# Performance work log

Measured on AMD Instinct MI355X. Metric: run time of the kernel, lower is better.

## Reference

```python
import jax, jax.numpy as jnp
import numpy as np

B, S, IN, OUT = 16, 512, 1024, 4096
QMAX = 127.0

def setup_inputs() -> dict:
    key = jax.random.key(0)
    k1, k2, k3, k4 = jax.random.split(key, 4)
    x = jax.random.normal(k1, (B, S, IN), dtype=jnp.float32)
    # int8 weights stored as int32 spec but clamped to int8 range, cast to int8
    weight_int8 = jax.random.randint(k2, (OUT, IN), -128, 128, dtype=jnp.int32).astype(jnp.int8)
    weight_scale = jax.random.uniform(k3, (OUT,), dtype=jnp.float32, minval=1e-4, maxval=0.02)
    bias = jax.random.normal(k4, (OUT,), dtype=jnp.float32)
    return {"x": x, "weight_int8": weight_int8, "weight_scale": weight_scale, "bias": bias}

def reference(x, weight_int8, weight_scale, bias):
    # dynamic per-token abs-max quantization
    abs_max = jnp.max(jnp.abs(x), axis=-1, keepdims=True)          # [B,S,1]
    input_scale = abs_max / QMAX
    input_scale = jnp.where(input_scale == 0, 1.0, input_scale)
    x_int8 = jnp.clip(jnp.round(x / input_scale), -128.0, 127.0)   # float-emulated int8
    # int8 matmul emulated in float (as in the original F.linear on .float())
    out_i32 = jnp.einsum('bsi,oi->bso', x_int8, weight_int8.astype(jnp.float32))
    out = out_i32 * weight_scale * input_scale                     # dequantize
    out = out + bias
    return out
```

## Files before the change

kernel.cpp:

```cpp
#include <hip/hip_runtime.h>


#define M_TOT 8192
#define N_TOT 4096
#define K_TOT 1024
#define QMAXF 127.0f

#define BM 256
#define BN 256
#define BK 128
#define NKT (K_TOT / BK)

typedef int i32x4 __attribute__((ext_vector_type(4)));

__global__ __launch_bounds__(256) void prep(const float* __restrict__ x,
                                            const int* __restrict__ w32,
                                            signed char* __restrict__ xq,
                                            signed char* __restrict__ w8,
                                            float* __restrict__ iscale) {
  const int b = blockIdx.x;
  const int t = threadIdx.x;

  if (b < M_TOT) {
    const float4 v = reinterpret_cast<const float4*>(x)[(size_t)b * 256 + t];
    float m = fmaxf(fmaxf(fabsf(v.x), fabsf(v.y)), fmaxf(fabsf(v.z), fabsf(v.w)));
#pragma unroll
    for (int off = 32; off >= 1; off >>= 1) m = fmaxf(m, __shfl_xor(m, off, 64));

    __shared__ float wmax[4];
    const int lane = t & 63, wid = t >> 6;
    if (lane == 0) wmax[wid] = m;
    __syncthreads();
    const float amax = fmaxf(fmaxf(wmax[0], wmax[1]), fmaxf(wmax[2], wmax[3]));

    float scale = amax / QMAXF;
    if (scale == 0.0f) scale = 1.0f;

    int qi;
    signed char* qb = reinterpret_cast<signed char*>(&qi);
    qb[0] = (signed char)(int)fminf(fmaxf(rintf(v.x / scale), -128.0f), 127.0f);
    qb[1] = (signed char)(int)fminf(fmaxf(rintf(v.y / scale), -128.0f), 127.0f);
    qb[2] = (signed char)(int)fminf(fmaxf(rintf(v.z / scale), -128.0f), 127.0f);
    qb[3] = (signed char)(int)fminf(fmaxf(rintf(v.w / scale), -128.0f), 127.0f);
    reinterpret_cast<int*>(xq)[(size_t)b * 256 + t] = qi;

    if (t == 0) iscale[b] = scale;
  } else {
    const int i = (b - M_TOT) * 256 + t;
    const int4 v = reinterpret_cast<const int4*>(w32)[i];
    const int packed = (v.x & 0xFF) | ((v.y & 0xFF) << 8) |
                       ((v.z & 0xFF) << 16) | (v.w << 24);
    reinterpret_cast<int*>(w8)[i] = packed;
  }
}

__device__ __forceinline__ void gload_lds16(const void* g, void* l) {
  __builtin_amdgcn_global_load_lds(
      (const __attribute__((address_space(1))) unsigned int*)g,
      (__attribute__((address_space(3))) unsigned int*)l, 16, 0, 0);
}

__global__ __launch_bounds__(512, 2) void int8_gemm(const signed char* __restrict__ xq,
                                                    const signed char* __restrict__ w,
                                                    const float* __restrict__ iscale,
                                                    const float* __restrict__ wscale,
                                                    const float* __restrict__ bias,
                                                    float* __restrict__ out) {
  __shared__ __attribute__((aligned(16))) signed char As[2][BM][BK];
  __shared__ __attribute__((aligned(16))) signed char Bs[2][BN][BK];

  const int t = threadIdx.x;
  const int lane = t & 63;
  const int wid = t >> 6;
  const int wm = wid >> 2;
  const int wn = wid & 3;

  const int bid = blockIdx.x;
  const int swz = (bid & 7) * 64 + (bid >> 3);
  const int m0 = (swz >> 4) * BM;
  const int n0 = (swz & 15) * BN;

  const int srow = t >> 3;
  const int scol_swz = ((t & 7) * 16) ^ ((srow & 7) << 4);

  auto stage = [&](int buf, int kt) {
    const int k0 = kt * BK;
#pragma unroll
    for (int c = 0; c < 4; ++c) {
      gload_lds16(xq + (size_t)(m0 + c * 64 + srow) * K_TOT + k0 + scol_swz,
                  &As[buf][c * 64][0] + t * 16);
      gload_lds16(w + (size_t)(n0 + c * 64 + srow) * K_TOT + k0 + scol_swz,
                  &Bs[buf][c * 64][0] + t * 16);
    }
  };

  i32x4 acc[8][4] = {};

  stage(0, 0);
  __syncthreads();

  for (int kt = 0; kt < NKT; ++kt) {
    const int cur = kt & 1;
    if (kt + 1 < NKT) stage(cur ^ 1, kt + 1);

#pragma unroll
    for (int ks = 0; ks < 2; ++ks) {
      const int kofs = ks * 64 + ((lane >> 4) * 16);
      i32x4 a[8], b[4];
#pragma unroll
      for (int f = 0; f < 8; ++f) {
        const int r = wm * 128 + f * 16 + (lane & 15);
        a[f] = *reinterpret_cast<const i32x4*>(&As[cur][r][kofs ^ ((r & 7) << 4)]);
      }
#pragma unroll
      for (int g = 0; g < 4; ++g) {
        const int r = wn * 64 + g * 16 + (lane & 15);
        b[g] = *reinterpret_cast<const i32x4*>(&Bs[cur][r][kofs ^ ((r & 7) << 4)]);
      }
#pragma unroll
      for (int f = 0; f < 8; ++f)
#pragma unroll
        for (int g = 0; g < 4; ++g)
          acc[f][g] = __builtin_amdgcn_mfma_i32_16x16x64_i8(a[f], b[g], acc[f][g], 0, 0, 0);
    }
    __syncthreads();
  }

  const int col = lane & 15;
  const int rq = lane >> 4;
  float wsc[4], bv[4];
#pragma unroll
  for (int g = 0; g < 4; ++g) {
    const int gn = n0 + wn * 64 + g * 16 + col;
    wsc[g] = wscale[gn];
    bv[g] = bias[gn];
  }
#pragma unroll
  for (int f = 0; f < 8; ++f) {
    const int gmb = m0 + wm * 128 + f * 16 + rq * 4;
#pragma unroll
    for (int i = 0; i < 4; ++i) {
      const int gm = gmb + i;
      const float isc = iscale[gm];
      float* rowp = out + (size_t)gm * N_TOT + n0 + wn * 64 + col;
#pragma unroll
      for (int g = 0; g < 4; ++g)
        rowp[g * 16] = (float)acc[f][g][i] * wsc[g] * isc + bv[g];
    }
  }
}

extern "C" void kernel_launch(void* const* d_in, const int* in_sizes, int n_in,
                              void* d_out, int out_size, void* d_ws, size_t ws_size,
                              hipStream_t stream) {
  const float* x = (const float*)d_in[0];
  const int* w32 = (const int*)d_in[1];
  const float* wscale = (const float*)d_in[2];
  const float* bias = (const float*)d_in[3];
  float* out = (float*)d_out;

  signed char* xq = (signed char*)d_ws;
  float* iscale = (float*)((char*)d_ws + (size_t)M_TOT * K_TOT);
  signed char* w8 = (signed char*)((char*)d_ws + (size_t)M_TOT * K_TOT + M_TOT * 4);

  const int pack_blocks = (N_TOT * K_TOT / 4) / 256;
  prep<<<M_TOT + pack_blocks, 256, 0, stream>>>(x, w32, xq, w8, iscale);
  int8_gemm<<<dim3((M_TOT / BM) * (N_TOT / BN)), 512, 0, stream>>>(xq, w8, iscale, wscale, bias, out);
}
```

Measured before the change: 63.93 us.

## Drop LDS staging; load MFMA operands directly from global into registers

Replaces the LDS double-buffered 256x256 tile GEMM with a register-only scheme. Each wave loads its A/B fragments straight from global memory into registers, double-buffered across k-steps, with s_setprio around the MFMA bursts. Block tile becomes 128x256 with 4 waves, and the grid mapping is remapped per XCD. Output stores become nontemporal. This removes LDS traffic and barriers, but every wave loses operand sharing through LDS and relies on L1/L2 for reuse, which raises global load traffic.

```diff
diff --git a/kernel.cpp b/kernel.cpp
--- a/kernel.cpp
+++ b/kernel.cpp
@@ -5,11 +5,6 @@
 #define N_TOT 4096
 #define K_TOT 1024
 #define QMAXF 127.0f
-
-#define BM 256
-#define BN 256
-#define BK 128
-#define NKT (K_TOT / BK)
 
 typedef int i32x4 __attribute__((ext_vector_type(4)));
 
@@ -54,76 +49,54 @@
   }
 }
 
-__device__ __forceinline__ void gload_lds16(const void* g, void* l) {
-  __builtin_amdgcn_global_load_lds(
-      (const __attribute__((address_space(1))) unsigned int*)g,
-      (__attribute__((address_space(3))) unsigned int*)l, 16, 0, 0);
-}
+#define LOADK(A_, B_, kt)                                                      \
+  _Pragma("unroll") for (int f = 0; f < 8; ++f)                                \
+      A_[f] = *reinterpret_cast<const i32x4*>(Abase + f * 16 * K_TOT + (kt) * 64); \
+  _Pragma("unroll") for (int g = 0; g < 4; ++g)                                \
+      B_[g] = *reinterpret_cast<const i32x4*>(Bbase + g * 16 * K_TOT + (kt) * 64);
 
-__global__ __launch_bounds__(512, 2) void int8_gemm(const signed char* __restrict__ xq,
+#define MFMAS(A_, B_)                                                          \
+  __builtin_amdgcn_s_setprio(1);                                               \
+  _Pragma("unroll") for (int f = 0; f < 8; ++f)                                \
+  _Pragma("unroll") for (int g = 0; g < 4; ++g)                                \
+      acc[f][g] = __builtin_amdgcn_mfma_i32_16x16x64_i8(A_[f], B_[g],          \
+                                                        acc[f][g], 0, 0, 0);   \
+  __builtin_amdgcn_s_setprio(0);
+
+__global__ __launch_bounds__(256, 2) void int8_gemm(const signed char* __restrict__ xq,
                                                     const signed char* __restrict__ w,
                                                     const float* __restrict__ iscale,
                                                     const float* __restrict__ wscale,
                                                     const float* __restrict__ bias,
                                                     float* __restrict__ out) {
-  __shared__ __attribute__((aligned(16))) signed char As[2][BM][BK];
-  __shared__ __attribute__((aligned(16))) signed char Bs[2][BN][BK];
-
   const int t = threadIdx.x;
   const int lane = t & 63;
   const int wid = t >> 6;
-  const int wm = wid >> 2;
-  const int wn = wid & 3;
 
   const int bid = blockIdx.x;
-  const int swz = (bid & 7) * 64 + (bid >> 3);
-  const int m0 = (swz >> 4) * BM;
-  const int n0 = (swz & 15) * BN;
+  const int xcd = bid & 7, li = bid >> 3;
+  const int mt = (xcd >> 1) * 16 + (li >> 3);
+  const int nt = (xcd & 1) * 8 + (li & 7);
+  const int m0 = mt * 128;
+  const int n0 = nt * 256 + wid * 64;
 
-  const int srow = t >> 3;
-  const int scol_swz = ((t & 7) * 16) ^ ((srow & 7) << 4);
-
-  auto stage = [&](int buf, int kt) {
-    const int k0 = kt * BK;
-#pragma unroll
-    for (int c = 0; c < 4; ++c) {
-      gload_lds16(xq + (size_t)(m0 + c * 64 + srow) * K_TOT + k0 + scol_swz,
-                  &As[buf][c * 64][0] + t * 16);
-      gload_lds16(w + (size_t)(n0 + c * 64 + srow) * K_TOT + k0 + scol_swz,
-                  &Bs[buf][c * 64][0] + t * 16);
-    }
-  };
+  const int lr = lane & 15;
+  const int kq = (lane >> 4) * 16;
+  const signed char* Abase = xq + (size_t)(m0 + lr) * K_TOT + kq;
+  const signed char* Bbase = w + (size_t)(n0 + lr) * K_TOT + kq;
 
   i32x4 acc[8][4] = {};
+  i32x4 a0[8], b0[4], a1[8], b1[4];
 
-  stage(0, 0);
-  __syncthreads();
-
-  for (int kt = 0; kt < NKT; ++kt) {
-    const int cur = kt & 1;
-    if (kt + 1 < NKT) stage(cur ^ 1, kt + 1);
+  LOADK(a0, b0, 0)
+  LOADK(a1, b1, 1)
 
 #pragma unroll
-    for (int ks = 0; ks < 2; ++ks) {
-      const int kofs = ks * 64 + ((lane >> 4) * 16);
-      i32x4 a[8], b[4];
-#pragma unroll
-      for (int f = 0; f < 8; ++f) {
-        const int r = wm * 128 + f * 16 + (lane & 15);
-        a[f] = *reinterpret_cast<const i32x4*>(&As[cur][r][kofs ^ ((r & 7) << 4)]);
-      }
-#pragma unroll
-      for (int g = 0; g < 4; ++g) {
-        const int r = wn * 64 + g * 16 + (lane & 15);
-        b[g] = *reinterpret_cast<const i32x4*>(&Bs[cur][r][kofs ^ ((r & 7) << 4)]);
-      }
-#pragma unroll
-      for (int f = 0; f < 8; ++f)
-#pragma unroll
-        for (int g = 0; g < 4; ++g)
-          acc[f][g] = __builtin_amdgcn_mfma_i32_16x16x64_i8(a[f], b[g], acc[f][g], 0, 0, 0);
-    }
-    __syncthreads();
+  for (int kt = 0; kt < K_TOT / 64; kt += 2) {
+    MFMAS(a0, b0)
+    if (kt + 2 < K_TOT / 64) LOADK(a0, b0, kt + 2)
+    MFMAS(a1, b1)
+    if (kt + 3 < K_TOT / 64) LOADK(a1, b1, kt + 3)
   }
 
   const int col = lane & 15;
@@ -131,21 +104,22 @@
   float wsc[4], bv[4];
 #pragma unroll
   for (int g = 0; g < 4; ++g) {
-    const int gn = n0 + wn * 64 + g * 16 + col;
+    const int gn = n0 + g * 16 + col;
     wsc[g] = wscale[gn];
     bv[g] = bias[gn];
   }
 #pragma unroll
   for (int f = 0; f < 8; ++f) {
-    const int gmb = m0 + wm * 128 + f * 16 + rq * 4;
+    const int gmb = m0 + f * 16 + rq * 4;
 #pragma unroll
     for (int i = 0; i < 4; ++i) {
       const int gm = gmb + i;
       const float isc = iscale[gm];
-      float* rowp = out + (size_t)gm * N_TOT + n0 + wn * 64 + col;
+      float* rowp = out + (size_t)gm * N_TOT + n0 + col;
 #pragma unroll
       for (int g = 0; g < 4; ++g)
-        rowp[g * 16] = (float)acc[f][g][i] * wsc[g] * isc + bv[g];
+        __builtin_nontemporal_store((float)acc[f][g][i] * wsc[g] * isc + bv[g],
+                                    rowp + g * 16);
     }
   }
 }
@@ -165,5 +139,5 @@
 
   const int pack_blocks = (N_TOT * K_TOT / 4) / 256;
   prep<<<M_TOT + pack_blocks, 256, 0, stream>>>(x, w32, xq, w8, iscale);
-  int8_gemm<<<dim3((M_TOT / BM) * (N_TOT / BN)), 512, 0, stream>>>(xq, w8, iscale, wscale, bias, out);
+  int8_gemm<<<dim3((M_TOT / 128) * (N_TOT / 256)), 256, 0, stream>>>(xq, w8, iscale, wscale, bias, out);
 }
```

Result: slower. 118.4 us (+85.1%).

## Shrink GEMM tiles to 128x128x64 with XCD-aware block mapping and MFMA priority

Applied to the files above, without the earlier changes.

Reduces block tiles from 256x256x128 to 128x128x64 with 256-thread blocks and four blocks per CU. The LDS swizzle is adapted to 64-byte rows. Blocks are remapped so each XCD owns a contiguous region of M/N tiles, and wave priority is raised around the MFMA sequence. The aim is more resident waves and better latency hiding and L2 locality, at the cost of lower per-block data reuse and more global and LDS load traffic per output.

```diff
diff --git a/kernel.cpp b/kernel.cpp
--- a/kernel.cpp
+++ b/kernel.cpp
@@ -6,9 +6,9 @@
 #define K_TOT 1024
 #define QMAXF 127.0f
 
-#define BM 256
-#define BN 256
-#define BK 128
+#define BM 128
+#define BN 128
+#define BK 64
 #define NKT (K_TOT / BK)
 
 typedef int i32x4 __attribute__((ext_vector_type(4)));
@@ -60,7 +60,7 @@
       (__attribute__((address_space(3))) unsigned int*)l, 16, 0, 0);
 }
 
-__global__ __launch_bounds__(512, 2) void int8_gemm(const signed char* __restrict__ xq,
+__global__ __launch_bounds__(256, 4) void int8_gemm(const signed char* __restrict__ xq,
                                                     const signed char* __restrict__ w,
                                                     const float* __restrict__ iscale,
                                                     const float* __restrict__ wscale,
@@ -72,21 +72,22 @@
   const int t = threadIdx.x;
   const int lane = t & 63;
   const int wid = t >> 6;
-  const int wm = wid >> 2;
-  const int wn = wid & 3;
+  const int wm = wid >> 1;
+  const int wn = wid & 1;
 
   const int bid = blockIdx.x;
-  const int swz = (bid & 7) * 64 + (bid >> 3);
-  const int m0 = (swz >> 4) * BM;
-  const int n0 = (swz & 15) * BN;
+  const int xcd = bid & 7, li = bid >> 3;
+  const int mt = (xcd >> 1) * 16 + (li >> 4);
+  const int nt = (xcd & 1) * 16 + (li & 15);
+  const int m0 = mt * BM, n0 = nt * BN;
 
-  const int srow = t >> 3;
-  const int scol_swz = ((t & 7) * 16) ^ ((srow & 7) << 4);
+  const int srow = t >> 2;
+  const int scol_swz = ((t & 3) * 16) ^ (((srow >> 1) & 3) << 4);
 
   auto stage = [&](int buf, int kt) {
     const int k0 = kt * BK;
 #pragma unroll
-    for (int c = 0; c < 4; ++c) {
+    for (int c = 0; c < 2; ++c) {
       gload_lds16(xq + (size_t)(m0 + c * 64 + srow) * K_TOT + k0 + scol_swz,
                   &As[buf][c * 64][0] + t * 16);
       gload_lds16(w + (size_t)(n0 + c * 64 + srow) * K_TOT + k0 + scol_swz,
@@ -94,7 +95,18 @@
     }
   };
 
-  i32x4 acc[8][4] = {};
+  const int lr = lane & 15;
+  const int kq = (lane >> 4) * 16;
+  auto rdA = [&](int buf, int f) -> i32x4 {
+    const int r = wm * 64 + f * 16 + lr;
+    return *reinterpret_cast<const i32x4*>(&As[buf][r][kq ^ (((r >> 1) & 3) << 4)]);
+  };
+  auto rdB = [&](int buf, int g) -> i32x4 {
+    const int r = wn * 64 + g * 16 + lr;
+    return *reinterpret_cast<const i32x4*>(&Bs[buf][r][kq ^ (((r >> 1) & 3) << 4)]);
+  };
+
+  i32x4 acc[4][4] = {};
 
   stage(0, 0);
   __syncthreads();
@@ -103,26 +115,20 @@
     const int cur = kt & 1;
     if (kt + 1 < NKT) stage(cur ^ 1, kt + 1);
 
+    i32x4 a[4], b[4];
 #pragma unroll
-    for (int ks = 0; ks < 2; ++ks) {
-      const int kofs = ks * 64 + ((lane >> 4) * 16);
-      i32x4 a[8], b[4];
+    for (int f = 0; f < 4; ++f) a[f] = rdA(cur, f);
 #pragma unroll
-      for (int f = 0; f < 8; ++f) {
-        const int r = wm * 128 + f * 16 + (lane & 15);
-        a[f] = *reinterpret_cast<const i32x4*>(&As[cur][r][kofs ^ ((r & 7) << 4)]);
-      }
+    for (int g = 0; g < 4; ++g) b[g] = rdB(cur, g);
+
+    __builtin_amdgcn_s_setprio(1);
 #pragma unroll
-      for (int g = 0; g < 4; ++g) {
-        const int r = wn * 64 + g * 16 + (lane & 15);
-        b[g] = *reinterpret_cast<const i32x4*>(&Bs[cur][r][kofs ^ ((r & 7) << 4)]);
-      }
+    for (int f = 0; f < 4; ++f)
 #pragma unroll
-      for (int f = 0; f < 8; ++f)
-#pragma unroll
-        for (int g = 0; g < 4; ++g)
-          acc[f][g] = __builtin_amdgcn_mfma_i32_16x16x64_i8(a[f], b[g], acc[f][g], 0, 0, 0);
-    }
+      for (int g = 0; g < 4; ++g)
+        acc[f][g] = __builtin_amdgcn_mfma_i32_16x16x64_i8(a[f], b[g], acc[f][g], 0, 0, 0);
+    __builtin_amdgcn_s_setprio(0);
+
     __syncthreads();
   }
 
@@ -136,8 +142,8 @@
     bv[g] = bias[gn];
   }
 #pragma unroll
-  for (int f = 0; f < 8; ++f) {
-    const int gmb = m0 + wm * 128 + f * 16 + rq * 4;
+  for (int f = 0; f < 4; ++f) {
+    const int gmb = m0 + wm * 64 + f * 16 + rq * 4;
 #pragma unroll
     for (int i = 0; i < 4; ++i) {
       const int gm = gmb + i;
@@ -165,5 +171,5 @@
 
   const int pack_blocks = (N_TOT * K_TOT / 4) / 256;
   prep<<<M_TOT + pack_blocks, 256, 0, stream>>>(x, w32, xq, w8, iscale);
-  int8_gemm<<<dim3((M_TOT / BM) * (N_TOT / BN)), 512, 0, stream>>>(xq, w8, iscale, wscale, bias, out);
+  int8_gemm<<<dim3((M_TOT / BM) * (N_TOT / BN)), 256, 0, stream>>>(xq, w8, iscale, wscale, bias, out);
 }
```

After: 68.67 us. 1.07x slower.

## Interleave split-half LDS staging with MFMA quadrants in ping-pong pipelined GEMM loop

Applied to the files above, without the earlier changes.

Restructures the int8 GEMM main loop into a hand-scheduled pipeline. Global-to-LDS loads are split into A and B halves and interleaved with four MFMA quadrant batches, using explicit s_waitcnt vmcnt and s_barrier instead of __syncthreads. MFMA bursts run at raised wave priority via s_setprio. Warp-to-tile mapping changes to an interleaved layout (rows f*32+wm*16, cols g*64+wn*16), with the epilogue indexing updated to match. Register-double-buffered fragments (aE/aO, bC/bN) hide LDS read latency, at the cost of higher register pressure and fragile barrier/vmcnt correctness.

```diff
diff --git a/kernel.cpp b/kernel.cpp
--- a/kernel.cpp
+++ b/kernel.cpp
@@ -59,6 +59,29 @@
       (const __attribute__((address_space(1))) unsigned int*)g,
       (__attribute__((address_space(3))) unsigned int*)l, 16, 0, 0);
 }
+
+#define BARF asm volatile("s_barrier" ::: "memory")
+#define VMW(n) asm volatile("s_waitcnt vmcnt(" #n ")" ::: "memory")
+
+#define MFMA16(AS, BS, MH, NH)                                                \
+  __builtin_amdgcn_s_setprio(1);                                              \
+  _Pragma("unroll") for (int j = 0; j < 4; ++j)                               \
+  _Pragma("unroll") for (int jb = 0; jb < 2; ++jb)                            \
+  _Pragma("unroll") for (int ks = 0; ks < 2; ++ks)                            \
+      acc[(MH) * 4 + j][(NH) * 2 + jb] = __builtin_amdgcn_mfma_i32_16x16x64_i8( \
+          AS[j * 2 + ks], BS[jb * 2 + ks], acc[(MH) * 4 + j][(NH) * 2 + jb],  \
+          0, 0, 0);                                                           \
+  __builtin_amdgcn_s_setprio(0);
+
+#define RD_A8(DST, BUF, MH)                                                   \
+  _Pragma("unroll") for (int j = 0; j < 4; ++j)                               \
+  _Pragma("unroll") for (int ks = 0; ks < 2; ++ks)                            \
+      DST[j * 2 + ks] = rdA(BUF, (MH) * 4 + j, ks);
+
+#define RD_B4(DST, BUF, NH)                                                   \
+  _Pragma("unroll") for (int jb = 0; jb < 2; ++jb)                            \
+  _Pragma("unroll") for (int ks = 0; ks < 2; ++ks)                            \
+      DST[jb * 2 + ks] = rdB(BUF, (NH) * 2 + jb, ks);
 
 __global__ __launch_bounds__(512, 2) void int8_gemm(const signed char* __restrict__ xq,
                                                     const signed char* __restrict__ w,
@@ -83,47 +106,85 @@
   const int srow = t >> 3;
   const int scol_swz = ((t & 7) * 16) ^ ((srow & 7) << 4);
 
-  auto stage = [&](int buf, int kt) {
+  auto stA = [&](int buf, int kt, int h) {
     const int k0 = kt * BK;
 #pragma unroll
-    for (int c = 0; c < 4; ++c) {
-      gload_lds16(xq + (size_t)(m0 + c * 64 + srow) * K_TOT + k0 + scol_swz,
-                  &As[buf][c * 64][0] + t * 16);
-      gload_lds16(w + (size_t)(n0 + c * 64 + srow) * K_TOT + k0 + scol_swz,
-                  &Bs[buf][c * 64][0] + t * 16);
+    for (int cc = 0; cc < 2; ++cc) {
+      const int row = h * 128 + cc * 64 + srow;
+      gload_lds16(xq + (size_t)(m0 + row) * K_TOT + k0 + scol_swz,
+                  &As[buf][h * 128 + cc * 64][0] + t * 16);
     }
   };
+  auto stB = [&](int buf, int kt, int h) {
+    const int k0 = kt * BK;
+#pragma unroll
+    for (int cc = 0; cc < 2; ++cc) {
+      const int row = h * 128 + cc * 64 + srow;
+      gload_lds16(w + (size_t)(n0 + row) * K_TOT + k0 + scol_swz,
+                  &Bs[buf][h * 128 + cc * 64][0] + t * 16);
+    }
+  };
+
+  const int lr = lane & 15;
+  const int kq = (lane >> 4) * 16;
+  const int sx = (lr & 7) << 4;
+  auto rdA = [&](int buf, int f, int ks) -> i32x4 {
+    const int r = f * 32 + wm * 16 + lr;
+    return *reinterpret_cast<const i32x4*>(&As[buf][r][(ks * 64 + kq) ^ sx]);
+  };
+  auto rdB = [&](int buf, int g, int ks) -> i32x4 {
+    const int r = g * 64 + wn * 16 + lr;
+    return *reinterpret_cast<const i32x4*>(&Bs[buf][r][(ks * 64 + kq) ^ sx]);
+  };
 
   i32x4 acc[8][4] = {};
-
-  stage(0, 0);
-  __syncthreads();
-
-  for (int kt = 0; kt < NKT; ++kt) {
-    const int cur = kt & 1;
-    if (kt + 1 < NKT) stage(cur ^ 1, kt + 1);
-
-#pragma unroll
-    for (int ks = 0; ks < 2; ++ks) {
-      const int kofs = ks * 64 + ((lane >> 4) * 16);
-      i32x4 a[8], b[4];
-#pragma unroll
-      for (int f = 0; f < 8; ++f) {
-        const int r = wm * 128 + f * 16 + (lane & 15);
-        a[f] = *reinterpret_cast<const i32x4*>(&As[cur][r][kofs ^ ((r & 7) << 4)]);
-      }
-#pragma unroll
-      for (int g = 0; g < 4; ++g) {
-        const int r = wn * 64 + g * 16 + (lane & 15);
-        b[g] = *reinterpret_cast<const i32x4*>(&Bs[cur][r][kofs ^ ((r & 7) << 4)]);
-      }
-#pragma unroll
-      for (int f = 0; f < 8; ++f)
-#pragma unroll
-        for (int g = 0; g < 4; ++g)
-          acc[f][g] = __builtin_amdgcn_mfma_i32_16x16x64_i8(a[f], b[g], acc[f][g], 0, 0, 0);
-    }
-    __syncthreads();
+  i32x4 aE[8], aO[8], bC[4], bN[4];
+
+  stA(0, 0, 0);
+  stB(0, 0, 0);
+  stB(0, 0, 1);
+  stA(0, 0, 1);
+  VMW(4); BARF;
+  RD_A8(aE, 0, 0)
+  RD_B4(bC, 0, 0)
+  VMW(2); BARF;
+
+  for (int U = 0; U < NKT - 1; ++U) {
+    const int c = U & 1, nb = c ^ 1;
+    RD_B4(bN, c, 1)
+    stA(nb, U + 1, 0);
+    BARF;
+    MFMA16(aE, bC, 0, 0)
+    VMW(2); BARF;
+    RD_A8(aO, c, 1)
+    stB(nb, U + 1, 0);
+    BARF;
+    MFMA16(aE, bN, 0, 1)
+    BARF;
+    stB(nb, U + 1, 1);
+    BARF;
+    MFMA16(aO, bC, 1, 0)
+    VMW(2); BARF;
+    RD_A8(aE, nb, 0)
+    RD_B4(bC, nb, 0)
+    stA(nb, U + 1, 1);
+    BARF;
+    MFMA16(aO, bN, 1, 1)
+    VMW(2); BARF;
+  }
+
+  {
+    const int c = (NKT - 1) & 1;
+    RD_B4(bN, c, 1)
+    BARF;
+    MFMA16(aE, bC, 0, 0)
+    VMW(0); BARF;
+    RD_A8(aO, c, 1)
+    BARF;
+    MFMA16(aE, bN, 0, 1)
+    BARF;
+    MFMA16(aO, bC, 1, 0)
+    MFMA16(aO, bN, 1, 1)
   }
 
   const int col = lane & 15;
@@ -131,21 +192,21 @@
   float wsc[4], bv[4];
 #pragma unroll
   for (int g = 0; g < 4; ++g) {
-    const int gn = n0 + wn * 64 + g * 16 + col;
+    const int gn = n0 + g * 64 + wn * 16 + col;
     wsc[g] = wscale[gn];
     bv[g] = bias[gn];
   }
 #pragma unroll
   for (int f = 0; f < 8; ++f) {
-    const int gmb = m0 + wm * 128 + f * 16 + rq * 4;
+    const int gmb = m0 + f * 32 + wm * 16 + rq * 4;
 #pragma unroll
     for (int i = 0; i < 4; ++i) {
       const int gm = gmb + i;
       const float isc = iscale[gm];
-      float* rowp = out + (size_t)gm * N_TOT + n0 + wn * 64 + col;
+      float* rowp = out + (size_t)gm * N_TOT + n0 + wn * 16 + col;
 #pragma unroll
       for (int g = 0; g < 4; ++g)
-        rowp[g * 16] = (float)acc[f][g][i] * wsc[g] * isc + bv[g];
+        rowp[g * 64] = (float)acc[f][g][i] * wsc[g] * isc + bv[g];
     }
   }
 }
```

Measured after the change: 65.55 us. +2.5%, slower.
